# Kernel tuning notes

Measured on AMD Instinct MI355X. Metric: run time of the kernel, lower is better.

The kernel has to match this reference:

```python
import jax, jax.numpy as jnp
import numpy as np

ALPHA = 0.2  # LeakyReLU negative slope
NEG_INF = -9e15  # matches torch's -9000000000000000.0
F_OUT = 64


def setup_inputs() -> dict:
    key = jax.random.key(0)
    k1, k2, k3, k4 = jax.random.split(key, 4)
    B, N, F_in = 8, 2048, 256
    h = jax.random.normal(k1, (B, N, F_in), dtype=jnp.float32)
    W = jax.random.normal(k2, (F_OUT, F_in), dtype=jnp.float32) * (1.0 / np.sqrt(F_in))
    a = jax.random.normal(k3, (2 * F_OUT, 1), dtype=jnp.float32)
    adj = jax.random.randint(k4, (B, N, N), 0, 2, dtype=jnp.int32)
    return {"h": h, "W": W, "a": a, "adj": adj}


def reference(h, W, a, adj):
    # Wh = Linear(h): [B, N, F_out]
    Wh = jnp.einsum("bnf,of->bno", h, W)
    # attention logits: e_ij = leakyrelu(Wh_i . a1 + Wh_j . a2)
    Wh1 = Wh @ a[:F_OUT]          # [B, N, 1]
    Wh2 = Wh @ a[F_OUT:]          # [B, N, 1]
    e = jax.nn.leaky_relu(Wh1 + jnp.swapaxes(Wh2, 1, 2), negative_slope=ALPHA)  # [B, N, N]
    att = jnp.where(adj > 0, e, NEG_INF)
    att = jax.nn.softmax(att, axis=2)
    # dropout is identity in eval mode
    h_prime = jnp.einsum("bnm,bmo->bno", att, Wh)
    return jax.nn.elu(h_prime)  # concat=True path
```

## Files before the change

### kernel.cpp

```cpp
#include <hip/hip_runtime.h>
#include <hip/hip_bf16.h>
#include <stdint.h>


typedef __attribute__((ext_vector_type(8))) short short8;
typedef __attribute__((ext_vector_type(4))) float f32x4;

#define GAT_ALPHA 0.2f

__device__ __forceinline__ short f2bf(float x) {
  union { float f; uint32_t u; } v; v.f = x;
  uint32_t r = v.u + 0x7FFFu + ((v.u >> 16) & 1u);
  return (short)(r >> 16);
}

__global__ __launch_bounds__(256) void k_wh(
    const float* __restrict__ h, const float* __restrict__ W,
    const float* __restrict__ a, short* __restrict__ whf,
    float* __restrict__ wh1, float* __restrict__ wh2)
{
  __shared__ float hl[32 * 132];
  __shared__ float Wl[64 * 132];
  const int tid  = threadIdx.x;
  const int og   = tid & 15;
  const int rg   = tid >> 4;
  const int row0 = blockIdx.x << 5;

  float acc[2][4] = {};

  for (int kp = 0; kp < 2; ++kp) {
    if (kp) __syncthreads();
#pragma unroll
    for (int i = 0; i < 4; ++i) {
      int idx4 = tid + (i << 8);
      int row = idx4 >> 5, kc = idx4 & 31;
      *(float4*)&hl[row * 132 + kc * 4] =
          *(const float4*)&h[(size_t)(row0 + row) * 256 + (kp << 7) + kc * 4];
    }
#pragma unroll
    for (int i = 0; i < 8; ++i) {
      int idx4 = tid + (i << 8);
      int o = idx4 >> 5, kc = idx4 & 31;
      *(float4*)&Wl[o * 132 + kc * 4] =
          *(const float4*)&W[o * 256 + (kp << 7) + kc * 4];
    }
    __syncthreads();
#pragma unroll 4
    for (int kc = 0; kc < 32; ++kc) {
      const int k0 = kc * 4;
      const float4 hv0 = *(const float4*)&hl[(rg * 2 + 0) * 132 + k0];
      const float4 hv1 = *(const float4*)&hl[(rg * 2 + 1) * 132 + k0];
#pragma unroll
      for (int c = 0; c < 4; ++c) {
        const float4 wv = *(const float4*)&Wl[(og + (c << 4)) * 132 + k0];
        acc[0][c] += hv0.x * wv.x + hv0.y * wv.y + hv0.z * wv.z + hv0.w * wv.w;
        acc[1][c] += hv1.x * wv.x + hv1.y * wv.y + hv1.z * wv.z + hv1.w * wv.w;
      }
    }
  }

  float a1v[4], a2v[4];
#pragma unroll
  for (int c = 0; c < 4; ++c) {
    a1v[c] = a[og + (c << 4)];
    a2v[c] = a[64 + og + (c << 4)];
  }
#pragma unroll
  for (int r = 0; r < 2; ++r) {
    const int row = row0 + rg * 2 + r;
    const int bb = row >> 11, j = row & 2047;
    const int s = j >> 5, g2 = (j >> 3) & 3, t = j & 7;
    const size_t base = ((size_t)bb << 17) +
                        (size_t)((s * 256 + g2 * 16 + og) * 8 + t);
    float p1 = 0.f, p2 = 0.f;
#pragma unroll
    for (int c = 0; c < 4; ++c) {
      whf[base + c * 512] = f2bf(acc[r][c]);
      p1 += acc[r][c] * a1v[c];
      p2 += acc[r][c] * a2v[c];
    }
#pragma unroll
    for (int off = 8; off; off >>= 1) {
      p1 += __shfl_xor(p1, off);
      p2 += __shfl_xor(p2, off);
    }
    if (og == 0) { wh1[row] = p1; wh2[row] = p2; }
  }
}

__global__ __launch_bounds__(256) void k_attn(
    const int* __restrict__ adj, const short* __restrict__ whf,
    const float* __restrict__ wh1, const float* __restrict__ wh2,
    float* __restrict__ out)
{
  const int blk = blockIdx.x;
  const int b   = blk >> 6;
  const int i0  = (blk & 63) << 5;
  const int tid = threadIdx.x;
  const int wave = tid >> 6;
  const int lane = tid & 63;
  const int og = lane & 15;
  const int g  = lane >> 4;
  const int rr  = (wave & 1) << 4;
  const int otb = (wave >> 1) << 1;

  __shared__ __align__(16) float wh2_l[2048];
  __shared__ float redm[4];

  float mp = -3.0e38f;
  const float* w2g = wh2 + (b << 11);
#pragma unroll
  for (int i = 0; i < 2; ++i) {
    const int idx4 = tid + (i << 8);
    const float4 v = *(const float4*)&w2g[idx4 << 2];
    *(float4*)&wh2_l[idx4 << 2] = v;
    mp = fmaxf(mp, fmaxf(fmaxf(v.x, v.y), fmaxf(v.z, v.w)));
  }
#pragma unroll
  for (int off = 32; off; off >>= 1) mp = fmaxf(mp, __shfl_xor(mp, off));
  if (lane == 0) redm[wave] = mp;
  __syncthreads();
  const float M2 = fmaxf(fmaxf(redm[0], redm[1]), fmaxf(redm[2], redm[3]));

  const int irow = i0 + rr + og;
  const float w1 = wh1[(b << 11) + irow];
  const float cm = w1 + M2;
  const float C  = fmaxf(cm, GAT_ALPHA * cm);

  const int* __restrict__ arow =
      adj + ((size_t)((b << 11) + irow) << 11) + (g << 3);
  const short8* __restrict__ fb = (const short8*)whf + (b << 14);

  f32x4 acc0 = {0.f, 0.f, 0.f, 0.f};
  f32x4 acc1 = {0.f, 0.f, 0.f, 0.f};
  float lsum = 0.f;

  int4 A0 = *(const int4*)arow;
  int4 A1 = *(const int4*)(arow + 4);
  short8 B0 = fb[otb * 64 + lane];
  short8 B1 = fb[(otb + 1) * 64 + lane];

  auto step = [&](const int4 cA0, const int4 cA1, const short8 cB0,
                  const short8 cB1, const int s) {
    const float4 wa = *(const float4*)&wh2_l[(s << 5) + (g << 3)];
    const float4 wb = *(const float4*)&wh2_l[(s << 5) + (g << 3) + 4];
    short8 af;
    float e, lk, p;
#define PCOMP(T, WV, AV)                                  \
    e = w1 + (WV); lk = fmaxf(e, GAT_ALPHA * e);          \
    p = __expf(lk - C); p = ((AV) > 0) ? p : 0.f;         \
    lsum += p; af[T] = f2bf(p);
    PCOMP(0, wa.x, cA0.x) PCOMP(1, wa.y, cA0.y)
    PCOMP(2, wa.z, cA0.z) PCOMP(3, wa.w, cA0.w)
    PCOMP(4, wb.x, cA1.x) PCOMP(5, wb.y, cA1.y)
    PCOMP(6, wb.z, cA1.z) PCOMP(7, wb.w, cA1.w)
#undef PCOMP
    acc0 = __builtin_amdgcn_mfma_f32_16x16x32_bf16(af, cB0, acc0, 0, 0, 0);
    acc1 = __builtin_amdgcn_mfma_f32_16x16x32_bf16(af, cB1, acc1, 0, 0, 0);
  };

  for (int s = 0; s < 63; ++s) {
    const int* an = arow + ((s + 1) << 5);
    const int4 nA0 = *(const int4*)an;
    const int4 nA1 = *(const int4*)(an + 4);
    const int fo = ((s + 1) << 2) + otb;
    const short8 nB0 = fb[fo * 64 + lane];
    const short8 nB1 = fb[(fo + 1) * 64 + lane];
    step(A0, A1, B0, B1, s);
    A0 = nA0; A1 = nA1; B0 = nB0; B1 = nB1;
  }
  step(A0, A1, B0, B1, 63);

  lsum += __shfl_xor(lsum, 16);
  lsum += __shfl_xor(lsum, 32);

#pragma unroll
  for (int q = 0; q < 4; ++q) {
    const float lq = __shfl(lsum, (g << 2) + q);
    const float rinv = 1.0f / lq;
    const int orow = i0 + rr + (g << 2) + q;
    float v0 = acc0[q] * rinv;
    float v1 = acc1[q] * rinv;
    v0 = v0 > 0.f ? v0 : __expf(v0) - 1.0f;
    v1 = v1 > 0.f ? v1 : __expf(v1) - 1.0f;
    const size_t ob = ((size_t)((b << 11) + orow)) << 6;
    out[ob + (otb << 4) + og] = v0;
    out[ob + ((otb + 1) << 4) + og] = v1;
  }
}

extern "C" void kernel_launch(void* const* d_in, const int* in_sizes, int n_in,
                              void* d_out, int out_size, void* d_ws,
                              size_t ws_size, hipStream_t stream) {
  (void)in_sizes; (void)n_in; (void)out_size; (void)ws_size;
  const float* h  = (const float*)d_in[0];
  const float* W  = (const float*)d_in[1];
  const float* a  = (const float*)d_in[2];
  const int* adj  = (const int*)d_in[3];
  float* out = (float*)d_out;

  short* whf = (short*)d_ws;
  float* wh1 = (float*)((char*)d_ws + 2 * 1024 * 1024);
  float* wh2 = wh1 + 8 * 2048;

  k_wh<<<512, 256, 0, stream>>>(h, W, a, whf, wh1, wh2);
  k_attn<<<512, 256, 0, stream>>>(adj, whf, wh1, wh2, out);
}
```

Before: 238.9 us.

## Split attention over j across waves and precompute per-column exponentials

Each block now handles 16 rows, with each wave covering a quarter of the neighbour range for all 64 output columns. Partial accumulators and row sums are combined through shared memory at the end. This removes the duplicate adjacency reads that came from splitting waves by output columns. The softmax numerator is rewritten as the max of two products of precomputed exponentials, which removes per-element exp from the inner loop. The cost is an LDS reduction, more accumulator registers, and a slightly different rounding path.

```diff
diff --git a/kernel.cpp b/kernel.cpp
--- a/kernel.cpp
+++ b/kernel.cpp
@@ -94,27 +94,28 @@
     float* __restrict__ out)
 {
   const int blk = blockIdx.x;
-  const int b   = blk >> 6;
-  const int i0  = (blk & 63) << 5;
+  const int b   = blk >> 7;
+  const int i0  = (blk & 127) << 4;
   const int tid = threadIdx.x;
   const int wave = tid >> 6;
   const int lane = tid & 63;
   const int og = lane & 15;
   const int g  = lane >> 4;
-  const int rr  = (wave & 1) << 4;
-  const int otb = (wave >> 1) << 1;
-
-  __shared__ __align__(16) float wh2_l[2048];
+
+  __shared__ __align__(16) float2 pn[2048];
+  __shared__ float lred[64];
   __shared__ float redm[4];
 
+  const float* w2g = wh2 + (b << 11);
+  float w2r[8];
   float mp = -3.0e38f;
-  const float* w2g = wh2 + (b << 11);
-#pragma unroll
-  for (int i = 0; i < 2; ++i) {
-    const int idx4 = tid + (i << 8);
-    const float4 v = *(const float4*)&w2g[idx4 << 2];
-    *(float4*)&wh2_l[idx4 << 2] = v;
-    mp = fmaxf(mp, fmaxf(fmaxf(v.x, v.y), fmaxf(v.z, v.w)));
+  {
+    const float4 v0 = *(const float4*)&w2g[tid << 3];
+    const float4 v1 = *(const float4*)&w2g[(tid << 3) + 4];
+    w2r[0] = v0.x; w2r[1] = v0.y; w2r[2] = v0.z; w2r[3] = v0.w;
+    w2r[4] = v1.x; w2r[5] = v1.y; w2r[6] = v1.z; w2r[7] = v1.w;
+#pragma unroll
+    for (int t = 0; t < 8; ++t) mp = fmaxf(mp, w2r[t]);
   }
 #pragma unroll
   for (int off = 32; off; off >>= 1) mp = fmaxf(mp, __shfl_xor(mp, off));
@@ -122,70 +123,114 @@
   __syncthreads();
   const float M2 = fmaxf(fmaxf(redm[0], redm[1]), fmaxf(redm[2], redm[3]));
 
-  const int irow = i0 + rr + og;
+  {
+    float4 st[4];
+#pragma unroll
+    for (int t = 0; t < 4; ++t) {
+      st[t].x = __expf(w2r[2 * t] - M2);
+      st[t].y = __expf(GAT_ALPHA * (w2r[2 * t] - M2));
+      st[t].z = __expf(w2r[2 * t + 1] - M2);
+      st[t].w = __expf(GAT_ALPHA * (w2r[2 * t + 1] - M2));
+    }
+#pragma unroll
+    for (int t = 0; t < 4; ++t)
+      *(float4*)&pn[(tid << 3) + 2 * t] = st[t];
+  }
+
+  const int irow = i0 + og;
   const float w1 = wh1[(b << 11) + irow];
   const float cm = w1 + M2;
   const float C  = fmaxf(cm, GAT_ALPHA * cm);
-
+  const float P1 = __expf(cm - C);
+  const float N1 = __expf(GAT_ALPHA * cm - C);
+  __syncthreads();
+
+  const int jbase0 = wave << 9;
   const int* __restrict__ arow =
-      adj + ((size_t)((b << 11) + irow) << 11) + (g << 3);
+      adj + ((size_t)((b << 11) + irow) << 11) + jbase0 + (g << 3);
   const short8* __restrict__ fb = (const short8*)whf + (b << 14);
-
-  f32x4 acc0 = {0.f, 0.f, 0.f, 0.f};
-  f32x4 acc1 = {0.f, 0.f, 0.f, 0.f};
+  const float4* __restrict__ pn4 = (const float4*)pn;
+  const int pnb = ((jbase0 >> 1) + (g << 2));
+  const int fo0 = (jbase0 >> 5) << 2;
+
+  f32x4 acc[4] = {{0.f,0.f,0.f,0.f},{0.f,0.f,0.f,0.f},
+                  {0.f,0.f,0.f,0.f},{0.f,0.f,0.f,0.f}};
   float lsum = 0.f;
 
   int4 A0 = *(const int4*)arow;
   int4 A1 = *(const int4*)(arow + 4);
-  short8 B0 = fb[otb * 64 + lane];
-  short8 B1 = fb[(otb + 1) * 64 + lane];
+  short8 B0 = fb[(fo0 + 0) * 64 + lane];
+  short8 B1 = fb[(fo0 + 1) * 64 + lane];
+  short8 B2 = fb[(fo0 + 2) * 64 + lane];
+  short8 B3 = fb[(fo0 + 3) * 64 + lane];
+
+  union Frag { short8 s; __hip_bfloat162 h[4]; };
 
   auto step = [&](const int4 cA0, const int4 cA1, const short8 cB0,
-                  const short8 cB1, const int s) {
-    const float4 wa = *(const float4*)&wh2_l[(s << 5) + (g << 3)];
-    const float4 wb = *(const float4*)&wh2_l[(s << 5) + (g << 3) + 4];
-    short8 af;
-    float e, lk, p;
-#define PCOMP(T, WV, AV)                                  \
-    e = w1 + (WV); lk = fmaxf(e, GAT_ALPHA * e);          \
-    p = __expf(lk - C); p = ((AV) > 0) ? p : 0.f;         \
-    lsum += p; af[T] = f2bf(p);
-    PCOMP(0, wa.x, cA0.x) PCOMP(1, wa.y, cA0.y)
-    PCOMP(2, wa.z, cA0.z) PCOMP(3, wa.w, cA0.w)
-    PCOMP(4, wb.x, cA1.x) PCOMP(5, wb.y, cA1.y)
-    PCOMP(6, wb.z, cA1.z) PCOMP(7, wb.w, cA1.w)
-#undef PCOMP
-    acc0 = __builtin_amdgcn_mfma_f32_16x16x32_bf16(af, cB0, acc0, 0, 0, 0);
-    acc1 = __builtin_amdgcn_mfma_f32_16x16x32_bf16(af, cB1, acc1, 0, 0, 0);
+                  const short8 cB1, const short8 cB2, const short8 cB3,
+                  const int s) {
+    const float4 q0 = pn4[pnb + (s << 4) + 0];
+    const float4 q1 = pn4[pnb + (s << 4) + 1];
+    const float4 q2 = pn4[pnb + (s << 4) + 2];
+    const float4 q3 = pn4[pnb + (s << 4) + 3];
+    float p[8];
+    p[0] = fmaxf(P1 * q0.x, N1 * q0.y); p[1] = fmaxf(P1 * q0.z, N1 * q0.w);
+    p[2] = fmaxf(P1 * q1.x, N1 * q1.y); p[3] = fmaxf(P1 * q1.z, N1 * q1.w);
+    p[4] = fmaxf(P1 * q2.x, N1 * q2.y); p[5] = fmaxf(P1 * q2.z, N1 * q2.w);
+    p[6] = fmaxf(P1 * q3.x, N1 * q3.y); p[7] = fmaxf(P1 * q3.z, N1 * q3.w);
+    p[0] = (cA0.x > 0) ? p[0] : 0.f;  p[1] = (cA0.y > 0) ? p[1] : 0.f;
+    p[2] = (cA0.z > 0) ? p[2] : 0.f;  p[3] = (cA0.w > 0) ? p[3] : 0.f;
+    p[4] = (cA1.x > 0) ? p[4] : 0.f;  p[5] = (cA1.y > 0) ? p[5] : 0.f;
+    p[6] = (cA1.z > 0) ? p[6] : 0.f;  p[7] = (cA1.w > 0) ? p[7] : 0.f;
+    lsum += ((p[0] + p[1]) + (p[2] + p[3])) + ((p[4] + p[5]) + (p[6] + p[7]));
+    Frag af;
+#pragma unroll
+    for (int t = 0; t < 4; ++t)
+      af.h[t] = __float22bfloat162_rn(float2{p[2 * t], p[2 * t + 1]});
+    acc[0] = __builtin_amdgcn_mfma_f32_16x16x32_bf16(af.s, cB0, acc[0], 0, 0, 0);
+    acc[1] = __builtin_amdgcn_mfma_f32_16x16x32_bf16(af.s, cB1, acc[1], 0, 0, 0);
+    acc[2] = __builtin_amdgcn_mfma_f32_16x16x32_bf16(af.s, cB2, acc[2], 0, 0, 0);
+    acc[3] = __builtin_amdgcn_mfma_f32_16x16x32_bf16(af.s, cB3, acc[3], 0, 0, 0);
   };
 
-  for (int s = 0; s < 63; ++s) {
+  for (int s = 0; s < 15; ++s) {
     const int* an = arow + ((s + 1) << 5);
     const int4 nA0 = *(const int4*)an;
     const int4 nA1 = *(const int4*)(an + 4);
-    const int fo = ((s + 1) << 2) + otb;
-    const short8 nB0 = fb[fo * 64 + lane];
+    const int fo = fo0 + ((s + 1) << 2);
+    const short8 nB0 = fb[(fo + 0) * 64 + lane];
     const short8 nB1 = fb[(fo + 1) * 64 + lane];
-    step(A0, A1, B0, B1, s);
-    A0 = nA0; A1 = nA1; B0 = nB0; B1 = nB1;
-  }
-  step(A0, A1, B0, B1, 63);
+    const short8 nB2 = fb[(fo + 2) * 64 + lane];
+    const short8 nB3 = fb[(fo + 3) * 64 + lane];
+    step(A0, A1, B0, B1, B2, B3, s);
+    A0 = nA0; A1 = nA1; B0 = nB0; B1 = nB1; B2 = nB2; B3 = nB3;
+  }
+  step(A0, A1, B0, B1, B2, B3, 15);
 
   lsum += __shfl_xor(lsum, 16);
   lsum += __shfl_xor(lsum, 32);
-
+  if (g == 0) lred[(wave << 4) + og] = lsum;
+
+  __syncthreads();
+  float* red = (float*)pn;
+#pragma unroll
+  for (int ot = 0; ot < 4; ++ot)
+#pragma unroll
+    for (int q = 0; q < 4; ++q)
+      red[(wave << 10) + ((g << 2) + q) * 64 + (ot << 4) + og] = acc[ot][q];
+  __syncthreads();
+
+  const int col = tid & 63;
+  const int rb  = tid >> 6;
 #pragma unroll
   for (int q = 0; q < 4; ++q) {
-    const float lq = __shfl(lsum, (g << 2) + q);
-    const float rinv = 1.0f / lq;
-    const int orow = i0 + rr + (g << 2) + q;
-    float v0 = acc0[q] * rinv;
-    float v1 = acc1[q] * rinv;
-    v0 = v0 > 0.f ? v0 : __expf(v0) - 1.0f;
-    v1 = v1 > 0.f ? v1 : __expf(v1) - 1.0f;
-    const size_t ob = ((size_t)((b << 11) + orow)) << 6;
-    out[ob + (otb << 4) + og] = v0;
-    out[ob + ((otb + 1) << 4) + og] = v1;
+    const int row = (rb << 2) + q;
+    float s = red[row * 64 + col] + red[1024 + row * 64 + col] +
+              red[2048 + row * 64 + col] + red[3072 + row * 64 + col];
+    const float l = lred[row] + lred[16 + row] + lred[32 + row] + lred[48 + row];
+    float v = s / l;
+    v = v > 0.f ? v : __expf(v) - 1.0f;
+    out[((size_t)((b << 11) + i0 + row) << 6) + col] = v;
   }
 }
 
@@ -204,5 +249,5 @@
   float* wh2 = wh1 + 8 * 2048;
 
   k_wh<<<512, 256, 0, stream>>>(h, W, a, whf, wh1, wh2);
-  k_attn<<<512, 256, 0, stream>>>(adj, whf, wh1, wh2, out);
-}
+  k_attn<<<1024, 256, 0, stream>>>(adj, whf, wh1, wh2, out);
+}
```

Measured after the change: 223.1 us, median of 2. 1.07x faster.
